# Kernel tuning notes

Hardware: AMD Instinct MI355X
Metric: run time of the kernel (lower is better)

Reference implementation:

```python
import jax, jax.numpy as jnp
import numpy as np

N_HEAD = 12
LN_EPS = 1e-5


def _layernorm(x, g, b):
    m = jnp.mean(x, axis=-1, keepdims=True)
    v = jnp.mean(jnp.square(x - m), axis=-1, keepdims=True)
    return (x - m) * jax.lax.rsqrt(v + LN_EPS) * g + b


def _block(x, p):
    # p holds single-layer params. x: [B, S, D]
    B, S, D = x.shape
    Dh = D // N_HEAD
    h = _layernorm(x, p['ln1_g'], p['ln1_b'])
    q = (h @ p['wq'] + p['bq']).reshape(B, S, N_HEAD, Dh)
    k = (h @ p['wk'] + p['bk']).reshape(B, S, N_HEAD, Dh)
    v = (h @ p['wv'] + p['bv']).reshape(B, S, N_HEAD, Dh)
    scores = jnp.einsum('bqhd,bkhd->bhqk', q, k) / np.sqrt(Dh).astype(x.dtype)
    causal = jnp.tril(jnp.ones((S, S), dtype=bool))  # valid_nums = arange(1..S)
    scores = jnp.where(causal, scores, -jnp.inf)
    attn = jax.nn.softmax(scores, axis=-1)  # dropout is identity in eval
    o = jnp.einsum('bhqk,bkhd->bqhd', attn, v).reshape(B, S, D)
    x = x + o @ p['wo'] + p['bo']
    h2 = _layernorm(x, p['ln2_g'], p['ln2_b'])
    ff = jax.nn.gelu(h2 @ p['w1'] + p['b1'], approximate=False) @ p['w2'] + p['b2']
    return x + ff


def _gpt_forward(idx, wte, wpe, layer_params, lnf_g, lnf_b, lm_w):
    S = idx.shape[1]
    x = wte[idx] + wpe[None, :S, :]  # embd dropout is identity in eval
    x = jax.lax.scan(lambda c, p: (_block(c, p), None), x, layer_params)[0]
    x = _layernorm(x, lnf_g, lnf_b)
    return x @ lm_w  # logits [B, S, V]


def setup_inputs() -> dict:
    B, S, D, V, L, F = 4, 1024, 768, 50257, 12, 3072
    key = jax.random.key(0)
    ks = iter(jax.random.split(key, 24))
    std = 0.02
    std_proj = 0.02 / np.sqrt(2 * L)  # special init for w_o / FFN.linear2

    def w(shape, s=std):
        return jax.random.normal(next(ks), shape, jnp.float32) * s

    return dict(
        idx=jax.random.randint(next(ks), (B, S), 0, V),
        wte=w((V, D)), wpe=w((S, D)),
        ln1_g=jnp.ones((L, D)), ln1_b=jnp.zeros((L, D)),
        wq=w((L, D, D)), bq=jnp.zeros((L, D)),
        wk=w((L, D, D)), bk=jnp.zeros((L, D)),
        wv=w((L, D, D)), bv=jnp.zeros((L, D)),
        wo=w((L, D, D), std_proj), bo=jnp.zeros((L, D)),
        ln2_g=jnp.ones((L, D)), ln2_b=jnp.zeros((L, D)),
        w1=w((L, D, F)), b1=jnp.zeros((L, F)),
        w2=w((L, F, D), std_proj), b2=jnp.zeros((L, D)),
        lnf_g=jnp.ones((D,)), lnf_b=jnp.zeros((D,)),
        lm_w=w((D, V)),
    )


def reference(idx, wte, wpe, ln1_g, ln1_b, wq, bq, wk, bk, wv, bv, wo, bo,
              ln2_g, ln2_b, w1, b1, w2, b2, lnf_g, lnf_b, lm_w):
    layer_params = dict(ln1_g=ln1_g, ln1_b=ln1_b, wq=wq, bq=bq, wk=wk, bk=bk,
                        wv=wv, bv=bv, wo=wo, bo=bo, ln2_g=ln2_g, ln2_b=ln2_b,
                        w1=w1, b1=b1, w2=w2, b2=b2)
    return _gpt_forward(idx, wte, wpe, layer_params, lnf_g, lnf_b, lm_w)
```

## Files before the change

kernel.cpp:

```cpp
#include <hip/hip_runtime.h>
#include <hip/hip_bf16.h>

typedef __attribute__((ext_vector_type(8))) short short8;
typedef __attribute__((ext_vector_type(4))) float floatx4;

#define GLD16(g, l) __builtin_amdgcn_global_load_lds( \
    (__attribute__((address_space(1))) void*)(g),      \
    (__attribute__((address_space(3))) void*)(l), 16, 0, 0)

#define MFMA_BF16(a, b, c) __builtin_amdgcn_mfma_f32_16x16x32_bf16((a), (b), (c), 0, 0, 0)

__device__ __forceinline__ short f2bf(float f) {
  union { __hip_bfloat16 h; short s; } u;
  u.h = __float2bfloat16(f);
  return u.s;
}

__global__ __launch_bounds__(256)
void transpose_convert(const float* __restrict__ in, short* __restrict__ out,
                       const int K, const int N, const size_t inStride,
                       const size_t outStride) {
  in += blockIdx.z * inStride;
  out += blockIdx.z * outStride;
  __shared__ float tile[32][33];
  const int n0 = blockIdx.x * 32;
  const int k0 = blockIdx.y * 32;
  const int tx = threadIdx.x;
  const int ty = threadIdx.y;
#pragma unroll
  for (int i = 0; i < 4; ++i) {
    const int kk = ty + i * 8;
    const int nn = n0 + tx;
    tile[kk][tx] = (nn < N) ? in[(size_t)(k0 + kk) * N + nn] : 0.f;
  }
  __syncthreads();
#pragma unroll
  for (int i = 0; i < 4; ++i) {
    const int nn = ty + i * 8;
    out[(size_t)(n0 + nn) * K + k0 + tx] = f2bf(tile[tx][nn]);
  }
}

__global__ __launch_bounds__(256)
void embed_kernel(const int* __restrict__ idx, const float* __restrict__ wte,
                  const float* __restrict__ wpe, float* __restrict__ x) {
  const int row = blockIdx.x;
  const int tok = idx[row];
  const int s = row & 1023;
  const float* wt = wte + (size_t)tok * 768;
  const float* wp = wpe + (size_t)s * 768;
  float* xr = x + (size_t)row * 768;
  for (int c = threadIdx.x; c < 768; c += 256) xr[c] = wt[c] + wp[c];
}

__global__ __launch_bounds__(256)
void ln_kernel(const float* __restrict__ x, const float* __restrict__ g,
               const float* __restrict__ b, short* __restrict__ out) {
  const int row = blockIdx.x;
  const int t = threadIdx.x;
  const int wv = t >> 6, lane = t & 63;
  const float* xr = x + (size_t)row * 768;
  const float v0 = xr[t], v1 = xr[t + 256], v2 = xr[t + 512];
  __shared__ float red[4];
  float s = v0 + v1 + v2;
#pragma unroll
  for (int m = 1; m < 64; m <<= 1) s += __shfl_xor(s, m);
  if (lane == 0) red[wv] = s;
  __syncthreads();
  const float mean = (red[0] + red[1] + red[2] + red[3]) * (1.0f / 768.0f);
  __syncthreads();
  const float d0 = v0 - mean, d1 = v1 - mean, d2 = v2 - mean;
  float q = d0 * d0 + d1 * d1 + d2 * d2;
#pragma unroll
  for (int m = 1; m < 64; m <<= 1) q += __shfl_xor(q, m);
  if (lane == 0) red[wv] = q;
  __syncthreads();
  const float var = (red[0] + red[1] + red[2] + red[3]) * (1.0f / 768.0f);
  const float inv = rsqrtf(var + 1e-5f);
  short* orow = out + (size_t)row * 768;
  orow[t] = f2bf(d0 * inv * g[t] + b[t]);
  orow[t + 256] = f2bf(d1 * inv * g[t + 256] + b[t + 256]);
  orow[t + 512] = f2bf(d2 * inv * g[t + 512] + b[t + 512]);
}

enum { EPI_QKV = 0, EPI_RESID = 1, EPI_GELU = 2 };

template <int BM, int EPI>
__global__ __launch_bounds__(256)
void gemm_kernel(const short* __restrict__ A, const short* __restrict__ Bt,
                 const int K,
                 const float* __restrict__ bias0, const float* __restrict__ bias1,
                 const float* __restrict__ bias2, float* __restrict__ fout,
                 short* __restrict__ bout0, short* __restrict__ bout1,
                 short* __restrict__ bout2) {
  constexpr int MF = BM / 32;
  constexpr int AR = BM / 64;
  __shared__ short sA[2][BM * 32];
  __shared__ short sB[2][64 * 32];
  const int tid = threadIdx.x;
  const int wv = tid >> 6;
  const int lane = tid & 63;
  const int lrow = lane & 15;
  const int lk8 = lane >> 4;
  const int m0 = blockIdx.x * BM;
  const int n0 = blockIdx.y * 64;
  const int wm = (wv >> 1) * (BM / 2);
  const int wn = (wv & 1) * 32;

  floatx4 acc[MF][2];
#pragma unroll
  for (int m = 0; m < MF; ++m)
#pragma unroll
    for (int n = 0; n < 2; ++n) acc[m][n] = {0.f, 0.f, 0.f, 0.f};

  const short* Ab = A + (size_t)m0 * K;
  const short* Bb = Bt + (size_t)n0 * K;

  const int nk = K >> 5;
#pragma unroll
  for (int i = 0; i < AR; ++i) {
    const int e = (i * 256 + tid) * 8;
    GLD16(Ab + (size_t)(e >> 5) * K + (e & 31), sA[0] + i * 2048 + wv * 512);
  }
  {
    const int e = tid * 8;
    GLD16(Bb + (size_t)(e >> 5) * K + (e & 31), sB[0] + wv * 512);
  }
  __syncthreads();

  int cur = 0;
  for (int kt = 0; kt < nk; ++kt) {
    if (kt + 1 < nk) {
      const int kb = (kt + 1) << 5;
#pragma unroll
      for (int i = 0; i < AR; ++i) {
        const int e = (i * 256 + tid) * 8;
        GLD16(Ab + (size_t)(e >> 5) * K + kb + (e & 31),
              sA[cur ^ 1] + i * 2048 + wv * 512);
      }
      const int e = tid * 8;
      GLD16(Bb + (size_t)(e >> 5) * K + kb + (e & 31), sB[cur ^ 1] + wv * 512);
    }
    short8 af[MF], bfv[2];
#pragma unroll
    for (int m = 0; m < MF; ++m)
      af[m] = *(const short8*)(sA[cur] + (wm + m * 16 + lrow) * 32 + lk8 * 8);
#pragma unroll
    for (int n = 0; n < 2; ++n)
      bfv[n] = *(const short8*)(sB[cur] + (wn + n * 16 + lrow) * 32 + lk8 * 8);
#pragma unroll
    for (int m = 0; m < MF; ++m)
#pragma unroll
      for (int n = 0; n < 2; ++n)
        acc[m][n] = MFMA_BF16(af[m], bfv[n], acc[m][n]);
    __syncthreads();
    cur ^= 1;
  }

#pragma unroll
  for (int m = 0; m < MF; ++m) {
#pragma unroll
    for (int n = 0; n < 2; ++n) {
#pragma unroll
      for (int r = 0; r < 4; ++r) {
        const float v = acc[m][n][r];
        const int gm = m0 + wm + m * 16 + lk8 * 4 + r;
        const int gn = n0 + wn + n * 16 + lrow;
        if (EPI == EPI_QKV) {
          const int sec = (gn >= 1536) ? 2 : (gn >= 768 ? 1 : 0);
          const int nn = gn - sec * 768;
          const int hh = nn >> 6, dh = nn & 63;
          const int bb = gm >> 10, srow = gm & 1023;
          if (sec == 0) {
            bout0[(((size_t)(bb * 12 + hh) * 1024 + srow) << 6) + dh] =
                f2bf((v + bias0[nn]) * 0.125f);
          } else if (sec == 1) {
            bout1[(((size_t)(bb * 12 + hh) * 1024 + srow) << 6) + dh] =
                f2bf(v + bias1[nn]);
          } else {
            bout2[(((size_t)(bb * 12 + hh) * 64 + dh) << 10) + srow] =
                f2bf(v + bias2[nn]);
          }
        } else if (EPI == EPI_RESID) {
          float* xp = fout + (size_t)gm * 768 + gn;
          *xp = *xp + v + bias0[gn];
        } else {
          const float tt = v + bias0[gn];
          const float gl = 0.5f * tt * (1.f + erff(tt * 0.70710678118654752f));
          bout0[(size_t)gm * 3072 + gn] = f2bf(gl);
        }
      }
    }
  }
}

__global__ __launch_bounds__(512)
void gemm_lm_kernel(const short* __restrict__ A, const short* __restrict__ Bt,
                    float* __restrict__ fout) {
  __shared__ short sA[2][256 * 32];
  __shared__ short sB[2][128 * 32];
  const int K = 768;
  const int tid = threadIdx.x;
  const int wv = tid >> 6;
  const int lane = tid & 63;
  const int lrow = lane & 15;
  const int lk8 = lane >> 4;
  const int m0 = blockIdx.x * 256;
  const int n0 = blockIdx.y * 128;
  const int wm = (wv >> 1) * 64;
  const int wn = (wv & 1) * 64;

  floatx4 acc[4][4];
#pragma unroll
  for (int m = 0; m < 4; ++m)
#pragma unroll
    for (int n = 0; n < 4; ++n) acc[m][n] = {0.f, 0.f, 0.f, 0.f};

  const int rA0 = tid >> 2, cA0 = (tid & 3) * 8;
  const int rA1 = 128 + (tid >> 2), cA1 = (tid & 3) * 8;
  const int rB = tid >> 2, cB = (tid & 3) * 8;

  const short* Ab = A + (size_t)m0 * K;
  const short* Bb = Bt + (size_t)n0 * K;

  GLD16(Ab + (size_t)rA0 * K + cA0, sA[0] + wv * 512);
  GLD16(Ab + (size_t)rA1 * K + cA1, sA[0] + 4096 + wv * 512);
  GLD16(Bb + (size_t)rB * K + cB, sB[0] + wv * 512);
  __syncthreads();

  int cur = 0;
  for (int kt = 0; kt < 24; ++kt) {
    if (kt + 1 < 24) {
      const int kb = (kt + 1) << 5;
      GLD16(Ab + (size_t)rA0 * K + kb + cA0, sA[cur ^ 1] + wv * 512);
      GLD16(Ab + (size_t)rA1 * K + kb + cA1, sA[cur ^ 1] + 4096 + wv * 512);
      GLD16(Bb + (size_t)rB * K + kb + cB, sB[cur ^ 1] + wv * 512);
    }
    short8 af[4], bfv[4];
#pragma unroll
    for (int m = 0; m < 4; ++m)
      af[m] = *(const short8*)(sA[cur] + (wm + m * 16 + lrow) * 32 + lk8 * 8);
#pragma unroll
    for (int n = 0; n < 4; ++n)
      bfv[n] = *(const short8*)(sB[cur] + (wn + n * 16 + lrow) * 32 + lk8 * 8);
#pragma unroll
    for (int m = 0; m < 4; ++m)
#pragma unroll
      for (int n = 0; n < 4; ++n)
        acc[m][n] = MFMA_BF16(af[m], bfv[n], acc[m][n]);
    __syncthreads();
    cur ^= 1;
  }

#pragma unroll
  for (int m = 0; m < 4; ++m)
#pragma unroll
    for (int n = 0; n < 4; ++n)
#pragma unroll
      for (int r = 0; r < 4; ++r) {
        const int gm = m0 + wm + m * 16 + lk8 * 4 + r;
        const int gn = n0 + wn + n * 16 + lrow;
        if (gn < 50257) fout[(size_t)gm * 50257 + gn] = acc[m][n][r];
      }
}

__global__ __launch_bounds__(256)
void attn_kernel(const short* __restrict__ q, const short* __restrict__ k,
                 const short* __restrict__ vt, short* __restrict__ o) {
  __shared__ short sK[64 * 64];
  __shared__ short sV[64 * 64];
  __shared__ short sP[4][16 * 64];
  const int bh = blockIdx.x;
  const int qi = 15 - blockIdx.y;
  const int tid = threadIdx.x;
  const int wv = tid >> 6, lane = tid & 63;
  const int lrow = lane & 15, lk8 = lane >> 4;
  const int q0 = qi * 64;

  const short* qg = q + ((size_t)(bh * 1024 + q0 + wv * 16 + lrow)) * 64 + lk8 * 8;
  const short8 qf0 = *(const short8*)qg;
  const short8 qf1 = *(const short8*)(qg + 32);

  float m_run[4], lsum[4];
  floatx4 accO[4];
#pragma unroll
  for (int r = 0; r < 4; ++r) { m_run[r] = -1e30f; lsum[r] = 0.f; }
#pragma unroll
  for (int n = 0; n < 4; ++n) accO[n] = {0.f, 0.f, 0.f, 0.f};

  for (int t = 0; t <= qi; ++t) {
    const int k0 = t * 64;
#pragma unroll
    for (int i = 0; i < 2; ++i) {
      const int e = (i * 256 + tid) * 8;
      const int r = e >> 6, cc = e & 63;
      const int su = ((cc >> 3) ^ (r & 7)) << 3;
      *(short8*)(sK + r * 64 + su) =
          *(const short8*)(k + ((size_t)(bh * 1024 + k0 + r)) * 64 + cc);
      *(short8*)(sV + r * 64 + su) =
          *(const short8*)(vt + ((size_t)(bh * 64 + r)) * 1024 + k0 + cc);
    }
    __syncthreads();

    floatx4 accS[4];
#pragma unroll
    for (int n = 0; n < 4; ++n) accS[n] = {0.f, 0.f, 0.f, 0.f};
#pragma unroll
    for (int ks = 0; ks < 2; ++ks) {
      const short8 qf = ks ? qf1 : qf0;
      const int u = lk8 + ks * 4;
#pragma unroll
      for (int n = 0; n < 4; ++n) {
        const int key = n * 16 + lrow;
        const short8 kf = *(const short8*)(sK + key * 64 + ((u ^ (key & 7)) << 3));
        accS[n] = MFMA_BF16(qf, kf, accS[n]);
      }
    }

#pragma unroll
    for (int r = 0; r < 4; ++r) {
      const int qrow = q0 + wv * 16 + lk8 * 4 + r;
      float sv[4];
      float mx = -1e30f;
#pragma unroll
      for (int n = 0; n < 4; ++n) {
        float s = accS[n][r];
        const int key = k0 + n * 16 + lrow;
        s = (key > qrow) ? -1e30f : s;
        sv[n] = s;
        mx = fmaxf(mx, s);
      }
#pragma unroll
      for (int m = 1; m < 16; m <<= 1) mx = fmaxf(mx, __shfl_xor(mx, m));
      const float mnew = fmaxf(m_run[r], mx);
      const float sf = __expf(m_run[r] - mnew);
      m_run[r] = mnew;
      float rs = 0.f;
      const int prow = lk8 * 4 + r;
#pragma unroll
      for (int n = 0; n < 4; ++n) {
        const float pv = __expf(sv[n] - mnew);
        rs += pv;
        const int col = n * 16 + lrow;
        sP[wv][prow * 64 + (((col >> 3) ^ (prow & 7)) << 3) + (col & 7)] = f2bf(pv);
      }
#pragma unroll
      for (int m = 1; m < 16; m <<= 1) rs += __shfl_xor(rs, m);
      lsum[r] = lsum[r] * sf + rs;
#pragma unroll
      for (int n = 0; n < 4; ++n) accO[n][r] *= sf;
    }

#pragma unroll
    for (int ks = 0; ks < 2; ++ks) {
      const int u = lk8 + ks * 4;
      const short8 pf =
          *(const short8*)(&sP[wv][lrow * 64 + ((u ^ (lrow & 7)) << 3)]);
#pragma unroll
      for (int n = 0; n < 4; ++n) {
        const int dh = n * 16 + lrow;
        const short8 vf = *(const short8*)(sV + dh * 64 + ((u ^ (dh & 7)) << 3));
        accO[n] = MFMA_BF16(pf, vf, accO[n]);
      }
    }
    __syncthreads();
  }

  const int bb = bh / 12, hh = bh % 12;
#pragma unroll
  for (int n = 0; n < 4; ++n)
#pragma unroll
    for (int r = 0; r < 4; ++r) {
      const int row = q0 + wv * 16 + lk8 * 4 + r;
      const float ov = accO[n][r] / lsum[r];
      o[((size_t)(bb * 1024 + row)) * 768 + hh * 64 + n * 16 + lrow] = f2bf(ov);
    }
}

extern "C" void kernel_launch(void* const* d_in, const int* in_sizes, int n_in,
                              void* d_out, int out_size, void* d_ws, size_t ws_size,
                              hipStream_t stream) {
  const int* idx = (const int*)d_in[0];
  const float* wte = (const float*)d_in[1];
  const float* wpe = (const float*)d_in[2];
  const float* ln1_g = (const float*)d_in[3];
  const float* ln1_b = (const float*)d_in[4];
  const float* wq = (const float*)d_in[5];
  const float* bq = (const float*)d_in[6];
  const float* wk = (const float*)d_in[7];
  const float* bk = (const float*)d_in[8];
  const float* wv = (const float*)d_in[9];
  const float* bv = (const float*)d_in[10];
  const float* wo = (const float*)d_in[11];
  const float* bo = (const float*)d_in[12];
  const float* ln2_g = (const float*)d_in[13];
  const float* ln2_b = (const float*)d_in[14];
  const float* w1 = (const float*)d_in[15];
  const float* b1 = (const float*)d_in[16];
  const float* w2 = (const float*)d_in[17];
  const float* b2 = (const float*)d_in[18];
  const float* lnf_g = (const float*)d_in[19];
  const float* lnf_b = (const float*)d_in[20];
  const float* lm_w = (const float*)d_in[21];
  float* out = (float*)d_out;

  char* base = (char*)d_ws;
  size_t off = 0;
  auto alloc = [&](size_t bytes) {
    char* r = base + off;
    off = (off + bytes + 255) & ~(size_t)255;
    return r;
  };
  short* lmT = (short*)alloc((size_t)50304 * 768 * 2);
  float* x = (float*)alloc((size_t)4096 * 768 * 4);
  short* h = (short*)alloc((size_t)4096 * 768 * 2);
  short* qb = (short*)alloc((size_t)4096 * 768 * 2);
  short* kb = (short*)alloc((size_t)4096 * 768 * 2);
  short* vtb = (short*)alloc((size_t)4096 * 768 * 2);
  short* ob = (short*)alloc((size_t)4096 * 768 * 2);
  short* ff = (short*)alloc((size_t)4096 * 3072 * 2);

  const size_t LW = 7077888;
  const size_t dd = (size_t)768 * 768;
  const bool big = (off + (size_t)12 * LW * 2 + 256 <= ws_size);
  short* wAll = nullptr;
  short *wqkvT = nullptr, *woT = nullptr, *w1T = nullptr, *w2T = nullptr;
  if (big) {
    wAll = (short*)alloc((size_t)12 * LW * 2);
  } else {
    wqkvT = (short*)alloc((size_t)2304 * 768 * 2);
    woT = (short*)alloc((size_t)768 * 768 * 2);
    w1T = (short*)alloc((size_t)3072 * 768 * 2);
    w2T = (short*)alloc((size_t)768 * 3072 * 2);
    if (off > ws_size) return;
  }

  const dim3 tb(32, 8);
  transpose_convert<<<dim3(1572, 24, 1), tb, 0, stream>>>(lm_w, lmT, 768, 50257, 0, 0);
  if (big) {
    transpose_convert<<<dim3(24, 24, 12), tb, 0, stream>>>(wq, wAll + 0, 768, 768, dd, LW);
    transpose_convert<<<dim3(24, 24, 12), tb, 0, stream>>>(wk, wAll + 589824, 768, 768, dd, LW);
    transpose_convert<<<dim3(24, 24, 12), tb, 0, stream>>>(wv, wAll + 1179648, 768, 768, dd, LW);
    transpose_convert<<<dim3(24, 24, 12), tb, 0, stream>>>(wo, wAll + 1769472, 768, 768, dd, LW);
    transpose_convert<<<dim3(96, 24, 12), tb, 0, stream>>>(w1, wAll + 2359296, 768, 3072,
                                                           (size_t)768 * 3072, LW);
    transpose_convert<<<dim3(24, 96, 12), tb, 0, stream>>>(w2, wAll + 4718592, 3072, 768,
                                                           (size_t)3072 * 768, LW);
  }
  embed_kernel<<<4096, 256, 0, stream>>>(idx, wte, wpe, x);

  for (int l = 0; l < 12; ++l) {
    const short *pQKV, *pWO, *pW1, *pW2;
    if (big) {
      short* wl = wAll + (size_t)l * LW;
      pQKV = wl;
      pWO = wl + 1769472;
      pW1 = wl + 2359296;
      pW2 = wl + 4718592;
    } else {
      transpose_convert<<<dim3(24, 24, 1), tb, 0, stream>>>(wq + l * dd, wqkvT, 768, 768, 0, 0);
      transpose_convert<<<dim3(24, 24, 1), tb, 0, stream>>>(wk + l * dd, wqkvT + dd, 768, 768, 0, 0);
      transpose_convert<<<dim3(24, 24, 1), tb, 0, stream>>>(wv + l * dd, wqkvT + 2 * dd, 768, 768, 0, 0);
      transpose_convert<<<dim3(24, 24, 1), tb, 0, stream>>>(wo + l * dd, woT, 768, 768, 0, 0);
      transpose_convert<<<dim3(96, 24, 1), tb, 0, stream>>>(w1 + (size_t)l * 768 * 3072, w1T, 768, 3072, 0, 0);
      transpose_convert<<<dim3(24, 96, 1), tb, 0, stream>>>(w2 + (size_t)l * 3072 * 768, w2T, 3072, 768, 0, 0);
      pQKV = wqkvT; pWO = woT; pW1 = w1T; pW2 = w2T;
    }

    ln_kernel<<<4096, 256, 0, stream>>>(x, ln1_g + l * 768, ln1_b + l * 768, h);
    gemm_kernel<128, EPI_QKV><<<dim3(32, 36), 256, 0, stream>>>(
        h, pQKV, 768, bq + l * 768, bk + l * 768, bv + l * 768, nullptr, qb, kb, vtb);
    attn_kernel<<<dim3(48, 16), 256, 0, stream>>>(qb, kb, vtb, ob);
    gemm_kernel<64, EPI_RESID><<<dim3(64, 12), 256, 0, stream>>>(
        ob, pWO, 768, bo + l * 768, nullptr, nullptr, x, nullptr, nullptr, nullptr);
    ln_kernel<<<4096, 256, 0, stream>>>(x, ln2_g + l * 768, ln2_b + l * 768, h);
    gemm_kernel<128, EPI_GELU><<<dim3(32, 48), 256, 0, stream>>>(
        h, pW1, 768, b1 + l * 3072, nullptr, nullptr, nullptr, ff, nullptr, nullptr);
    gemm_kernel<64, EPI_RESID><<<dim3(64, 12), 256, 0, stream>>>(
        ff, pW2, 3072, b2 + l * 768, nullptr, nullptr, x, nullptr, nullptr, nullptr);
  }

  ln_kernel<<<4096, 256, 0, stream>>>(x, lnf_g, lnf_b, h);
  gemm_lm_kernel<<<dim3(16, 393), 512, 0, stream>>>(h, lmT, out);
}
```

Before: 3.386 ms.

## Use 64-wide K tiles with XOR-swizzled LDS and reuse generic GEMM for LM head

The GEMM K tile is doubled from 32 to 64, which halves the number of main-loop iterations and barriers. Shared-memory staging now uses an XOR swizzle on the 16-byte chunk index, applied on the global source address of the direct-to-LDS loads and matched on the fragment reads, to cut LDS bank conflicts. The kernel gains a BN template parameter, and the dedicated 512-thread 256x128 LM-head kernel is replaced by the generic kernel with a 128x128 tile and an LM epilogue. This doubles LDS use per block and changes the LM-head tiling and occupancy, which could help or hurt that large GEMM.

```diff
diff --git a/kernel.cpp b/kernel.cpp
--- a/kernel.cpp
+++ b/kernel.cpp
@@ -83,9 +83,31 @@
   orow[t + 512] = f2bf(d2 * inv * g[t + 512] + b[t + 512]);
 }
 
-enum { EPI_QKV = 0, EPI_RESID = 1, EPI_GELU = 2 };
-
-template <int BM, int EPI>
+enum { EPI_QKV = 0, EPI_RESID = 1, EPI_GELU = 2, EPI_LM = 3 };
+
+template <int BM, int BN>
+__device__ __forceinline__ void stage_tiles(const short* __restrict__ Ab,
+                                            const short* __restrict__ Bb,
+                                            const int K, const int kb,
+                                            short* pa, short* pb,
+                                            const int tid, const int wv) {
+#pragma unroll
+  for (int i = 0; i < BM / 32; ++i) {
+    const int p = i * 256 + tid;
+    const int rr = p >> 3, up = p & 7;
+    GLD16(Ab + (size_t)rr * K + kb + ((up ^ (rr & 7)) << 3),
+          pa + (i * 256 + wv * 64) * 8);
+  }
+#pragma unroll
+  for (int i = 0; i < BN / 32; ++i) {
+    const int p = i * 256 + tid;
+    const int rr = p >> 3, up = p & 7;
+    GLD16(Bb + (size_t)rr * K + kb + ((up ^ (rr & 7)) << 3),
+          pb + (i * 256 + wv * 64) * 8);
+  }
+}
+
+template <int BM, int BN, int EPI>
 __global__ __launch_bounds__(256)
 void gemm_kernel(const short* __restrict__ A, const short* __restrict__ Bt,
                  const int K,
@@ -94,65 +116,59 @@
                  short* __restrict__ bout0, short* __restrict__ bout1,
                  short* __restrict__ bout2) {
   constexpr int MF = BM / 32;
-  constexpr int AR = BM / 64;
-  __shared__ short sA[2][BM * 32];
-  __shared__ short sB[2][64 * 32];
+  constexpr int NF = BN / 32;
+  __shared__ short sA[2][BM * 64];
+  __shared__ short sB[2][BN * 64];
   const int tid = threadIdx.x;
   const int wv = tid >> 6;
   const int lane = tid & 63;
   const int lrow = lane & 15;
   const int lk8 = lane >> 4;
   const int m0 = blockIdx.x * BM;
-  const int n0 = blockIdx.y * 64;
+  const int n0 = blockIdx.y * BN;
   const int wm = (wv >> 1) * (BM / 2);
-  const int wn = (wv & 1) * 32;
-
-  floatx4 acc[MF][2];
+  const int wn = (wv & 1) * (BN / 2);
+
+  floatx4 acc[MF][NF];
 #pragma unroll
   for (int m = 0; m < MF; ++m)
 #pragma unroll
-    for (int n = 0; n < 2; ++n) acc[m][n] = {0.f, 0.f, 0.f, 0.f};
+    for (int n = 0; n < NF; ++n) acc[m][n] = {0.f, 0.f, 0.f, 0.f};
 
   const short* Ab = A + (size_t)m0 * K;
   const short* Bb = Bt + (size_t)n0 * K;
 
-  const int nk = K >> 5;
-#pragma unroll
-  for (int i = 0; i < AR; ++i) {
-    const int e = (i * 256 + tid) * 8;
-    GLD16(Ab + (size_t)(e >> 5) * K + (e & 31), sA[0] + i * 2048 + wv * 512);
-  }
-  {
-    const int e = tid * 8;
-    GLD16(Bb + (size_t)(e >> 5) * K + (e & 31), sB[0] + wv * 512);
-  }
+  const int nk = K >> 6;
+  stage_tiles<BM, BN>(Ab, Bb, K, 0, sA[0], sB[0], tid, wv);
   __syncthreads();
 
   int cur = 0;
   for (int kt = 0; kt < nk; ++kt) {
-    if (kt + 1 < nk) {
-      const int kb = (kt + 1) << 5;
-#pragma unroll
-      for (int i = 0; i < AR; ++i) {
-        const int e = (i * 256 + tid) * 8;
-        GLD16(Ab + (size_t)(e >> 5) * K + kb + (e & 31),
-              sA[cur ^ 1] + i * 2048 + wv * 512);
-      }
-      const int e = tid * 8;
-      GLD16(Bb + (size_t)(e >> 5) * K + kb + (e & 31), sB[cur ^ 1] + wv * 512);
-    }
-    short8 af[MF], bfv[2];
+    if (kt + 1 < nk)
+      stage_tiles<BM, BN>(Ab, Bb, K, (kt + 1) << 6, sA[cur ^ 1], sB[cur ^ 1],
+                          tid, wv);
+    const short* pa = sA[cur];
+    const short* pb = sB[cur];
+    short8 af[MF][2], bv[NF][2];
 #pragma unroll
     for (int m = 0; m < MF; ++m)
-      af[m] = *(const short8*)(sA[cur] + (wm + m * 16 + lrow) * 32 + lk8 * 8);
-#pragma unroll
-    for (int n = 0; n < 2; ++n)
-      bfv[n] = *(const short8*)(sB[cur] + (wn + n * 16 + lrow) * 32 + lk8 * 8);
+#pragma unroll
+      for (int ks = 0; ks < 2; ++ks)
+        af[m][ks] = *(const short8*)(pa + (wm + m * 16 + lrow) * 64 +
+                                     (((ks * 4 + lk8) ^ (lrow & 7)) << 3));
+#pragma unroll
+    for (int n = 0; n < NF; ++n)
+#pragma unroll
+      for (int ks = 0; ks < 2; ++ks)
+        bv[n][ks] = *(const short8*)(pb + (wn + n * 16 + lrow) * 64 +
+                                     (((ks * 4 + lk8) ^ (lrow & 7)) << 3));
 #pragma unroll
     for (int m = 0; m < MF; ++m)
 #pragma unroll
-      for (int n = 0; n < 2; ++n)
-        acc[m][n] = MFMA_BF16(af[m], bfv[n], acc[m][n]);
+      for (int n = 0; n < NF; ++n) {
+        acc[m][n] = MFMA_BF16(af[m][0], bv[n][0], acc[m][n]);
+        acc[m][n] = MFMA_BF16(af[m][1], bv[n][1], acc[m][n]);
+      }
     __syncthreads();
     cur ^= 1;
   }
@@ -160,7 +176,7 @@
 #pragma unroll
   for (int m = 0; m < MF; ++m) {
 #pragma unroll
-    for (int n = 0; n < 2; ++n) {
+    for (int n = 0; n < NF; ++n) {
 #pragma unroll
       for (int r = 0; r < 4; ++r) {
         const float v = acc[m][n][r];
@@ -184,84 +200,16 @@
         } else if (EPI == EPI_RESID) {
           float* xp = fout + (size_t)gm * 768 + gn;
           *xp = *xp + v + bias0[gn];
-        } else {
+        } else if (EPI == EPI_GELU) {
           const float tt = v + bias0[gn];
           const float gl = 0.5f * tt * (1.f + erff(tt * 0.70710678118654752f));
           bout0[(size_t)gm * 3072 + gn] = f2bf(gl);
+        } else {
+          if (gn < 50257) fout[(size_t)gm * 50257 + gn] = v;
         }
       }
     }
   }
-}
-
-__global__ __launch_bounds__(512)
-void gemm_lm_kernel(const short* __restrict__ A, const short* __restrict__ Bt,
-                    float* __restrict__ fout) {
-  __shared__ short sA[2][256 * 32];
-  __shared__ short sB[2][128 * 32];
-  const int K = 768;
-  const int tid = threadIdx.x;
-  const int wv = tid >> 6;
-  const int lane = tid & 63;
-  const int lrow = lane & 15;
-  const int lk8 = lane >> 4;
-  const int m0 = blockIdx.x * 256;
-  const int n0 = blockIdx.y * 128;
-  const int wm = (wv >> 1) * 64;
-  const int wn = (wv & 1) * 64;
-
-  floatx4 acc[4][4];
-#pragma unroll
-  for (int m = 0; m < 4; ++m)
-#pragma unroll
-    for (int n = 0; n < 4; ++n) acc[m][n] = {0.f, 0.f, 0.f, 0.f};
-
-  const int rA0 = tid >> 2, cA0 = (tid & 3) * 8;
-  const int rA1 = 128 + (tid >> 2), cA1 = (tid & 3) * 8;
-  const int rB = tid >> 2, cB = (tid & 3) * 8;
-
-  const short* Ab = A + (size_t)m0 * K;
-  const short* Bb = Bt + (size_t)n0 * K;
-
-  GLD16(Ab + (size_t)rA0 * K + cA0, sA[0] + wv * 512);
-  GLD16(Ab + (size_t)rA1 * K + cA1, sA[0] + 4096 + wv * 512);
-  GLD16(Bb + (size_t)rB * K + cB, sB[0] + wv * 512);
-  __syncthreads();
-
-  int cur = 0;
-  for (int kt = 0; kt < 24; ++kt) {
-    if (kt + 1 < 24) {
-      const int kb = (kt + 1) << 5;
-      GLD16(Ab + (size_t)rA0 * K + kb + cA0, sA[cur ^ 1] + wv * 512);
-      GLD16(Ab + (size_t)rA1 * K + kb + cA1, sA[cur ^ 1] + 4096 + wv * 512);
-      GLD16(Bb + (size_t)rB * K + kb + cB, sB[cur ^ 1] + wv * 512);
-    }
-    short8 af[4], bfv[4];
-#pragma unroll
-    for (int m = 0; m < 4; ++m)
-      af[m] = *(const short8*)(sA[cur] + (wm + m * 16 + lrow) * 32 + lk8 * 8);
-#pragma unroll
-    for (int n = 0; n < 4; ++n)
-      bfv[n] = *(const short8*)(sB[cur] + (wn + n * 16 + lrow) * 32 + lk8 * 8);
-#pragma unroll
-    for (int m = 0; m < 4; ++m)
-#pragma unroll
-      for (int n = 0; n < 4; ++n)
-        acc[m][n] = MFMA_BF16(af[m], bfv[n], acc[m][n]);
-    __syncthreads();
-    cur ^= 1;
-  }
-
-#pragma unroll
-  for (int m = 0; m < 4; ++m)
-#pragma unroll
-    for (int n = 0; n < 4; ++n)
-#pragma unroll
-      for (int r = 0; r < 4; ++r) {
-        const int gm = m0 + wm + m * 16 + lk8 * 4 + r;
-        const int gn = n0 + wn + n * 16 + lrow;
-        if (gn < 50257) fout[(size_t)gm * 50257 + gn] = acc[m][n][r];
-      }
 }
 
 __global__ __launch_bounds__(256)
@@ -468,18 +416,19 @@
     }
 
     ln_kernel<<<4096, 256, 0, stream>>>(x, ln1_g + l * 768, ln1_b + l * 768, h);
-    gemm_kernel<128, EPI_QKV><<<dim3(32, 36), 256, 0, stream>>>(
+    gemm_kernel<128, 64, EPI_QKV><<<dim3(32, 36), 256, 0, stream>>>(
         h, pQKV, 768, bq + l * 768, bk + l * 768, bv + l * 768, nullptr, qb, kb, vtb);
     attn_kernel<<<dim3(48, 16), 256, 0, stream>>>(qb, kb, vtb, ob);
-    gemm_kernel<64, EPI_RESID><<<dim3(64, 12), 256, 0, stream>>>(
+    gemm_kernel<64, 64, EPI_RESID><<<dim3(64, 12), 256, 0, stream>>>(
         ob, pWO, 768, bo + l * 768, nullptr, nullptr, x, nullptr, nullptr, nullptr);
     ln_kernel<<<4096, 256, 0, stream>>>(x, ln2_g + l * 768, ln2_b + l * 768, h);
-    gemm_kernel<128, EPI_GELU><<<dim3(32, 48), 256, 0, stream>>>(
+    gemm_kernel<128, 64, EPI_GELU><<<dim3(32, 48), 256, 0, stream>>>(
         h, pW1, 768, b1 + l * 3072, nullptr, nullptr, nullptr, ff, nullptr, nullptr);
-    gemm_kernel<64, EPI_RESID><<<dim3(64, 12), 256, 0, stream>>>(
+    gemm_kernel<64, 64, EPI_RESID><<<dim3(64, 12), 256, 0, stream>>>(
         ff, pW2, 3072, b2 + l * 768, nullptr, nullptr, x, nullptr, nullptr, nullptr);
   }
 
   ln_kernel<<<4096, 256, 0, stream>>>(x, lnf_g, lnf_b, h);
-  gemm_lm_kernel<<<dim3(16, 393), 512, 0, stream>>>(h, lmT, out);
-}
+  gemm_kernel<128, 128, EPI_LM><<<dim3(32, 393), 256, 0, stream>>>(
+      h, lmT, 768, nullptr, nullptr, nullptr, out, nullptr, nullptr, nullptr);
+}
```

Result: faster. 3.271 ms (-3.4%).
